# Optimization experiments

Measured on AMD Instinct MI355X. Metric: run time of the kernel, lower is better.

Reference implementation:

```python
import jax, jax.numpy as jnp
import numpy as np

B, N, F, E, D, H, L = 4, 2048, 2, 16, 32, 4, 2
GRAPH_LAYERS = 3
FLOW_ITERS = 10
COST_C = 1.0        # quadratic cost: c*x^2, inv_derivative(y) = y/(2c)
BIG_NUMBER = 1e7


def setup_inputs():
    key = jax.random.key(0)
    ks = jax.random.split(key, 20)
    node_features = jax.random.normal(ks[0], (B, N, F), jnp.float32)
    node_embeddings = jax.random.normal(ks[1], (B, N, E), jnp.float32)
    demands = jax.random.normal(ks[2], (B, N, 1), jnp.float32)
    demands = demands - demands.mean(axis=1, keepdims=True)  # flow conservation
    adj = (jax.random.uniform(ks[3], (B, N, N)) < 0.01).astype(jnp.float32)
    adj = adj * (1.0 - jnp.eye(N, dtype=jnp.float32))
    eye = jnp.broadcast_to(jnp.eye(N, dtype=jnp.float32), (B, N, N))
    neighborhoods = jnp.stack([eye, adj], axis=1)  # [B,L,N,N] hop-0 and hop-1
    def g(k, shape):
        return jax.random.normal(k, shape, jnp.float32) * 0.1
    params = {
        'We1': g(ks[4], (E + F, D)), 'be1': jnp.zeros((D,), jnp.float32),
        'We2': g(ks[5], (D, D)), 'be2': jnp.zeros((D,), jnp.float32),
        'w_attn': g(ks[6], (H, D)),
        'Wo': g(ks[7], (D, D)), 'bo': jnp.zeros((D,), jnp.float32),
        'Wz': g(ks[8], (D, D)), 'Uz': g(ks[9], (D, D)), 'bz': jnp.zeros((D,), jnp.float32),
        'Wr': g(ks[10], (D, D)), 'Ur': g(ks[11], (D, D)), 'br': jnp.zeros((D,), jnp.float32),
        'Wh': g(ks[12], (D, D)), 'Uh': g(ks[13], (D, D)), 'bh': jnp.zeros((D,), jnp.float32),
        'Wd1': g(ks[14], (D, D)), 'bd1': jnp.zeros((D,), jnp.float32),
        'Wd2': g(ks[15], (D, 1)), 'bd2': jnp.zeros((1,), jnp.float32),
        'Wv1': g(ks[16], (D, D)), 'bv1': jnp.zeros((D,), jnp.float32),
        'Wv2': g(ks[17], (D, 1)), 'bv2': jnp.zeros((1,), jnp.float32),
    }
    return {'node_features': node_features, 'node_embeddings': node_embeddings,
            'demands': demands, 'adj': adj, 'neighborhoods': neighborhoods, **params}


def _forward(node_features, node_embeddings, demands, adj, neighborhoods,
             We1, be1, We2, be2, w_attn, Wo, bo,
             Wz, Uz, bz, Wr, Ur, br, Wh, Uh, bh,
             Wd1, bd1, Wd2, bd2, Wv1, bv1, Wv2, bv2):
    # --- node encoder MLP (tanh, activate_final=True) ---
    x = jnp.concatenate([node_embeddings, node_features], axis=-1)   # [B,N,E+F]
    enc = jnp.tanh(jnp.tanh(x @ We1 + be1) @ We2 + be2)               # [B,N,D]
    # row-normalized neighborhood operators (degree-normalized aggregation)
    Mnorm = neighborhoods / (jnp.sum(neighborhoods, axis=-1, keepdims=True) + 1.0)
    # --- graph_layers x (attention neighborhood + GRU state update) ---
    for _ in range(GRAPH_LAYERS):
        agg = jnp.einsum('blnm,bmd->blnd', Mnorm, enc)                # [B,L,N,D]
        scores = jnp.einsum('blnd,hd->bhnl', jnp.tanh(agg), w_attn)   # [B,H,N,L]
        alpha = jax.nn.softmax(scores, axis=-1)
        ctx = jnp.einsum('bhnl,blnd->bnd', alpha, agg) / H            # mean over heads
        nbr = jnp.tanh(ctx @ Wo + bo)                                 # [B,N,D]
        z = jax.nn.sigmoid(nbr @ Wz + enc @ Uz + bz)
        r = jax.nn.sigmoid(nbr @ Wr + enc @ Ur + br)
        h = jnp.tanh(nbr @ Wh + (r * enc) @ Uh + bh)
        enc = z * enc + (1.0 - z) * h
    # --- primal: edge weights, masked softmax, proportional flow solver ---
    pred = (enc @ Wd1 + bd1) @ Wd2 + bd2                              # [B,N,1]
    pw = pred * jnp.transpose(pred, (0, 2, 1))                        # [B,N,N]
    weights = -BIG_NUMBER * (1.0 - adj) + pw
    fwp = jax.nn.softmax(weights, axis=-1)                            # rows sum to 1
    flow0 = fwp * jax.nn.relu(-demands)

    def step(flow, _):
        inflow = jnp.sum(flow, axis=1)[..., None]                     # [B,N,1]
        return fwp * jax.nn.relu(inflow - demands), None

    flow, _ = jax.lax.scan(step, flow0, None, length=FLOW_ITERS)
    flow_cost = jnp.sum(COST_C * flow * flow, axis=(1, 2))            # [B]
    # --- dual: dual variables, dual flows via inverse cost derivative ---
    dual = (enc @ Wv1 + bv1) @ Wv2 + bv2                              # [B,N,1]
    dd = dual - jnp.transpose(dual, (0, 2, 1))                        # [B,N,N]
    df = adj * jax.nn.relu(dd / (2.0 * COST_C))
    dual_cost = jnp.sum(COST_C * df * df - dd * df, axis=(1, 2)) \
        - jnp.sum(dual * demands, axis=(1, 2))                        # [B]
    return flow_cost - dual_cost                                      # primal-dual gap loss, [B]


def reference(node_features, node_embeddings, demands, adj, neighborhoods,
              We1, be1, We2, be2, w_attn, Wo, bo,
              Wz, Uz, bz, Wr, Ur, br, Wh, Uh, bh,
              Wd1, bd1, Wd2, bd2, Wv1, bv1, Wv2, bv2):
    return _forward(node_features, node_embeddings, demands, adj, neighborhoods,
                    We1, be1, We2, be2, w_attn, Wo, bo,
                    Wz, Uz, bz, Wr, Ur, br, Wh, Uh, bh,
                    Wd1, bd1, Wd2, bd2, Wv1, bv1, Wv2, bv2)
```

## Files before the change

kernel.cpp:

```cpp
#include <hip/hip_runtime.h>

#define NN 2048
#define NB 4
#define BN (NB * NN)
#define MAXD 96

__device__ __forceinline__ float fast_rcp(float x) { return __builtin_amdgcn_rcpf(x); }
__device__ __forceinline__ float fast_tanh(float x) {
    float a = __expf(2.0f * fabsf(x));
    float r = 1.0f - 2.0f * fast_rcp(1.0f + a);
    return copysignf(r, x);
}
__device__ __forceinline__ float fast_sigmoid(float x) {
    return fast_rcp(1.0f + __expf(-x));
}

__global__ __launch_bounds__(256) void k_front(
    const float* __restrict__ feat, const float* __restrict__ emb,
    const float* __restrict__ We1, const float* __restrict__ be1,
    const float* __restrict__ We2, const float* __restrict__ be2,
    float* __restrict__ enc_out,
    const float* __restrict__ adj, int* __restrict__ deg, int* __restrict__ cols,
    int* __restrict__ tdeg)
{
    int tid = threadIdx.x;
    if (blockIdx.x < 1024) {
        __shared__ float sW1[18 * 32], sb1[32], sW2[32 * 32], sb2[32];
        for (int i = tid; i < 18 * 32; i += 256) sW1[i] = We1[i];
        for (int i = tid; i < 32 * 32; i += 256) sW2[i] = We2[i];
        if (tid < 32) { sb1[tid] = be1[tid]; sb2[tid] = be2[tid]; }
        __syncthreads();
        int group = tid >> 5, j = tid & 31;
        int node = blockIdx.x * 8 + group;
        float x;
        if (j < 16)      x = emb[node * 16 + j];
        else if (j < 18) x = feat[node * 2 + (j - 16)];
        else             x = 0.f;
        float acc = sb1[j];
#pragma unroll
        for (int k = 0; k < 18; k++)
            acc += __shfl(x, k, 32) * sW1[k * 32 + j];
        float h = fast_tanh(acc);
        float acc2 = sb2[j];
#pragma unroll
        for (int k = 0; k < 32; k++)
            acc2 += __shfl(h, k, 32) * sW2[k * 32 + j];
        enc_out[node * 32 + j] = fast_tanh(acc2);
    } else {
        int wave = tid >> 6, lane = tid & 63;
        int row = (blockIdx.x - 1024) * 4 + wave;
        const float4* p = (const float4*)(adj + (size_t)row * NN);
        int cnt = 0;
        int base = row * MAXD;
#pragma unroll
        for (int it = 0; it < 8; it++) {
            float4 v = p[it * 64 + lane];
            float va[4] = { v.x, v.y, v.z, v.w };
#pragma unroll
            for (int c = 0; c < 4; c++) {
                unsigned long long m = __ballot(va[c] != 0.f);
                if (va[c] != 0.f) {
                    int pos = cnt + __popcll(m & ((1ull << lane) - 1ull));
                    if (pos < MAXD) cols[base + pos] = it * 256 + lane * 4 + c;
                }
                cnt += __popcll(m);
            }
        }
        if (lane == 0) {
            deg[row] = cnt < MAXD ? cnt : MAXD;
            tdeg[row] = 0;
        }
    }
}

__device__ __forceinline__ float layer_rest(
    int g, int j, float e, float a1raw, int d,
    const float4* sPack, const float2* sWhUh, const float* sWo,
    const float* sAttn, const float* sbo, const float* sbz,
    const float* sbr, const float* sbh,
    float2 (*sNE)[32], float (*sCtx)[32])
{
    float agg0 = 0.5f * e;
    float a1 = a1raw * fast_rcp((float)(d + 1));
    float t0 = fast_tanh(agg0), t1 = fast_tanh(a1);
    float td = t0 - t1;
    float s0 = sAttn[j] * td, s1 = sAttn[32 + j] * td,
          s2 = sAttn[64 + j] * td, s3 = sAttn[96 + j] * td;
#pragma unroll
    for (int off = 16; off >= 1; off >>= 1) {
        s0 += __shfl_xor(s0, off, 32);
        s1 += __shfl_xor(s1, off, 32);
        s2 += __shfl_xor(s2, off, 32);
        s3 += __shfl_xor(s3, off, 32);
    }
    float c0 = 0.25f * (fast_sigmoid(s0) + fast_sigmoid(s1) +
                        fast_sigmoid(s2) + fast_sigmoid(s3));
    float ctx = c0 * agg0 + (1.0f - c0) * a1;
    sCtx[g][j] = ctx;
    float acc = sbo[j];
#pragma unroll
    for (int k = 0; k < 32; k++)
        acc += sCtx[g][k] * sWo[k * 32 + j];
    float nbr = fast_tanh(acc);
    sNE[g][j] = make_float2(nbr, e);
    float az = sbz[j], ar = sbr[j];
#pragma unroll
    for (int k = 0; k < 32; k++) {
        float2 ne = sNE[g][k];
        float4 w  = sPack[k * 32 + j];
        az += ne.x * w.x + ne.y * w.y;
        ar += ne.x * w.z + ne.y * w.w;
    }
    float z = fast_sigmoid(az), r = fast_sigmoid(ar);
    sNE[g][j].y = r * e;
    float ah = sbh[j];
#pragma unroll
    for (int k = 0; k < 32; k++) {
        float2 ne = sNE[g][k];
        float2 wh = sWhUh[k * 32 + j];
        ah += ne.x * wh.x + ne.y * wh.y;
    }
    float hc = fast_tanh(ah);
    return z * e + (1.0f - z) * hc;
}

__device__ __forceinline__ float hop1_gather(
    int g, int j, int d, const int* __restrict__ cp,
    const float* __restrict__ encB, int (*sCols)[64])
{
    sCols[g][j]      = cp[j];
    sCols[g][j + 32] = cp[j + 32];
    float a = 0.f, b = 0.f, c = 0.f, e4 = 0.f;
    int i = 0;
    for (; i + 3 < d; i += 4) {
        int m0 = sCols[g][i],     m1 = sCols[g][i + 1];
        int m2 = sCols[g][i + 2], m3 = sCols[g][i + 3];
        a  += encB[m0 * 32 + j];
        b  += encB[m1 * 32 + j];
        c  += encB[m2 * 32 + j];
        e4 += encB[m3 * 32 + j];
    }
    for (; i < d; i++) a += encB[sCols[g][i] * 32 + j];
    return (a + b) + (c + e4);
}

__global__ __launch_bounds__(1024) void k_layer(
    const float* __restrict__ enc_in, float* __restrict__ enc_out,
    const int* __restrict__ deg, const int* __restrict__ cols,
    const float* __restrict__ w_attn,
    const float* __restrict__ Wo, const float* __restrict__ bo,
    const float* __restrict__ Wz, const float* __restrict__ Uz, const float* __restrict__ bz,
    const float* __restrict__ Wr, const float* __restrict__ Ur, const float* __restrict__ br,
    const float* __restrict__ Wh, const float* __restrict__ Uh, const float* __restrict__ bh)
{
    __shared__ float4 sPack[1024];
    __shared__ float2 sWhUh[1024];
    __shared__ float  sWo[1024];
    __shared__ float  sAttn[128], sbo[32], sbz[32], sbr[32], sbh[32];
    __shared__ int    sCols[32][64];
    __shared__ float2 sNE[32][32];
    __shared__ float  sCtx[32][32];
    int tid = threadIdx.x;
    sPack[tid] = make_float4(Wz[tid], Uz[tid], Wr[tid], Ur[tid]);
    sWhUh[tid] = make_float2(Wh[tid], Uh[tid]);
    sWo[tid] = Wo[tid];
    if (tid < 128) sAttn[tid] = w_attn[tid];
    if (tid < 32) { sbo[tid] = bo[tid]; sbz[tid] = bz[tid]; sbr[tid] = br[tid]; sbh[tid] = bh[tid]; }
    int g = tid >> 5, j = tid & 31;
    int node = blockIdx.x * 32 + g;
    int b = node >> 11;
    const float* encB = enc_in + (size_t)(b * NN) * 32;
    float e = enc_in[node * 32 + j];
    int d = deg[node];
    const int* cp = cols + node * MAXD;
    float a1 = hop1_gather(g, j, d, cp, encB, sCols);
    __syncthreads();
    float eo = layer_rest(g, j, e, a1, d, sPack, sWhUh, sWo,
                          sAttn, sbo, sbz, sbr, sbh, sNE, sCtx);
    enc_out[node * 32 + j] = eo;
}

__global__ __launch_bounds__(1024) void k_layer_last(
    const float* __restrict__ enc_in,
    const int* __restrict__ deg, const int* __restrict__ cols,
    const float* __restrict__ w_attn,
    const float* __restrict__ Wo, const float* __restrict__ bo,
    const float* __restrict__ Wz, const float* __restrict__ Uz, const float* __restrict__ bz,
    const float* __restrict__ Wr, const float* __restrict__ Ur, const float* __restrict__ br,
    const float* __restrict__ Wh, const float* __restrict__ Uh, const float* __restrict__ bh,
    const float* __restrict__ Wd1, const float* __restrict__ bd1,
    const float* __restrict__ Wd2, const float* __restrict__ bd2,
    const float* __restrict__ Wv1, const float* __restrict__ bv1,
    const float* __restrict__ Wv2, const float* __restrict__ bv2,
    float* __restrict__ pred, float* __restrict__ dual)
{
    __shared__ float4 sPack[1024];
    __shared__ float2 sWhUh[1024];
    __shared__ float  sWo[1024];
    __shared__ float  sAttn[128], sbo[32], sbz[32], sbr[32], sbh[32];
    __shared__ float  swd[32], swv[32], shc[2];
    __shared__ int    sCols[32][64];
    __shared__ float2 sNE[32][32];
    __shared__ float  sCtx[32][32];
    int tid = threadIdx.x;
    sPack[tid] = make_float4(Wz[tid], Uz[tid], Wr[tid], Ur[tid]);
    sWhUh[tid] = make_float2(Wh[tid], Uh[tid]);
    sWo[tid] = Wo[tid];
    if (tid < 128) sAttn[tid] = w_attn[tid];
    if (tid < 32) { sbo[tid] = bo[tid]; sbz[tid] = bz[tid]; sbr[tid] = br[tid]; sbh[tid] = bh[tid]; }
    if (tid >= 64 && tid < 96) {
        int k = tid - 64;
        float a = 0.f, av = 0.f;
#pragma unroll
        for (int jj = 0; jj < 32; jj++) {
            a  += Wd1[k * 32 + jj] * Wd2[jj];
            av += Wv1[k * 32 + jj] * Wv2[jj];
        }
        swd[k] = a; swv[k] = av;
    }
    if (tid == 96) {
        float c1 = 0.f, c2 = 0.f;
#pragma unroll
        for (int jj = 0; jj < 32; jj++) {
            c1 += bd1[jj] * Wd2[jj];
            c2 += bv1[jj] * Wv2[jj];
        }
        shc[0] = c1 + bd2[0]; shc[1] = c2 + bv2[0];
    }
    int g = tid >> 5, j = tid & 31;
    int node = blockIdx.x * 32 + g;
    int b = node >> 11;
    const float* encB = enc_in + (size_t)(b * NN) * 32;
    float e = enc_in[node * 32 + j];
    int d = deg[node];
    const int* cp = cols + node * MAXD;
    float a1 = hop1_gather(g, j, d, cp, encB, sCols);
    __syncthreads();
    float eo = layer_rest(g, j, e, a1, d, sPack, sWhUh, sWo,
                          sAttn, sbo, sbz, sbr, sbh, sNE, sCtx);
    float pd = eo * swd[j];
    float dv = eo * swv[j];
#pragma unroll
    for (int off = 16; off >= 1; off >>= 1) {
        pd += __shfl_xor(pd, off, 32);
        dv += __shfl_xor(dv, off, 32);
    }
    if (j == 0) {
        pred[node] = pd + shc[0];
        dual[node] = dv + shc[1];
    }
}

__global__ __launch_bounds__(256) void k_edge_scatter(
    const int* __restrict__ deg, const int* __restrict__ cols,
    const float* __restrict__ pred, const float* __restrict__ dual,
    int* __restrict__ tdeg, unsigned* __restrict__ tpack,
    float* __restrict__ rowsq, float* __restrict__ rowdual)
{
    int wave = threadIdx.x >> 6, lane = threadIdx.x & 63;
    int row = blockIdx.x * 4 + wave;
    int b = row >> 11;
    int rloc = row & (NN - 1);
    const float* predB = pred + b * NN;
    const float* dualB = dual + b * NN;
    int d = deg[row];
    int base = row * MAXD;
    float pn = pred[row];
    float dn = dual[row];
    if (d <= 64) {
        int c = 0;
        float w = -1e30f, du = 0.f;
        bool act = lane < d;
        if (act) {
            c = cols[base + lane];
            w = pn * predB[c];
            float dd = dn - dualB[c];
            if (dd > 0.f) du = -0.25f * dd * dd;
        }
        float mx = w;
#pragma unroll
        for (int off = 32; off >= 1; off >>= 1) mx = fmaxf(mx, __shfl_xor(mx, off));
        float ex = act ? __expf(w - mx) : 0.f;
        float den = ex;
#pragma unroll
        for (int off = 32; off >= 1; off >>= 1) { den += __shfl_xor(den, off); du += __shfl_xor(du, off); }
        float f = ex * fast_rcp(den);
        float rs = f * f;
        if (act) {
            int pos = atomicAdd(&tdeg[b * NN + c], 1);
            if (pos < MAXD) {
                unsigned wv = ((__float_as_uint(f) + 0x400u) & 0xFFFFF800u) | (unsigned)rloc;
                tpack[(size_t)(b * MAXD + pos) * NN + c] = wv;
            }
        } else rs = 0.f;
#pragma unroll
        for (int off = 32; off >= 1; off >>= 1) rs += __shfl_xor(rs, off);
        if (lane == 0) { rowsq[row] = rs; rowdual[row] = du; }
    } else {
        float mx = -1e30f;
        for (int i = lane; i < d; i += 64) {
            int c = cols[base + i];
            mx = fmaxf(mx, pn * predB[c]);
        }
#pragma unroll
        for (int off = 32; off >= 1; off >>= 1) mx = fmaxf(mx, __shfl_xor(mx, off));
        float den = 0.f, du = 0.f;
        for (int i = lane; i < d; i += 64) {
            int c = cols[base + i];
            den += __expf(pn * predB[c] - mx);
            float dd = dn - dualB[c];
            if (dd > 0.f) du -= 0.25f * dd * dd;
        }
#pragma unroll
        for (int off = 32; off >= 1; off >>= 1) { den += __shfl_xor(den, off); du += __shfl_xor(du, off); }
        float invden = fast_rcp(den);
        float rs = 0.f;
        for (int i = lane; i < d; i += 64) {
            int c = cols[base + i];
            float f = __expf(pn * predB[c] - mx) * invden;
            rs += f * f;
            int pos = atomicAdd(&tdeg[b * NN + c], 1);
            if (pos < MAXD) {
                unsigned wv = ((__float_as_uint(f) + 0x400u) & 0xFFFFF800u) | (unsigned)rloc;
                tpack[(size_t)(b * MAXD + pos) * NN + c] = wv;
            }
        }
#pragma unroll
        for (int off = 32; off >= 1; off >>= 1) rs += __shfl_xor(rs, off);
        if (lane == 0) { rowsq[row] = rs; rowdual[row] = du; }
    }
}

__global__ __launch_bounds__(1024) void k_flow_batch(
    const int* __restrict__ tdeg, const unsigned* __restrict__ tpack,
    const float* __restrict__ demands,
    const float* __restrict__ rowsq, const float* __restrict__ rowdual,
    const float* __restrict__ dual, float* __restrict__ out)
{
    __shared__ float sdem[NN], sA[NN], sBuf[NN];
    __shared__ float red[3][16];
    int tid = threadIdx.x;
    int b = blockIdx.x;
    const float* demB = demands + b * NN;
    for (int n = tid; n < NN; n += 1024) {
        float dm = demB[n];
        sdem[n] = dm;
        sA[n] = fmaxf(-dm, 0.f);
    }
    __syncthreads();
    int n0 = tid, n1 = tid + 1024;
    int d0 = tdeg[b * NN + n0];
    int d1 = tdeg[b * NN + n1];
    if (d0 > MAXD) d0 = MAXD;
    if (d1 > MAXD) d1 = MAXD;
    float dm0 = sdem[n0], dm1 = sdem[n1];
    const unsigned* tp = tpack + (size_t)b * MAXD * NN;
#pragma unroll 1
    for (int it = 0; it < 5; it++) {
        {
            float a0 = 0.f, a1 = 0.f;
            for (int i = 0; i < d0; i++) {
                unsigned wv = tp[i * NN + n0];
                a0 += __uint_as_float(wv & 0xFFFFF800u) * sA[wv & 0x7FFu];
            }
            for (int i = 0; i < d1; i++) {
                unsigned wv = tp[i * NN + n1];
                a1 += __uint_as_float(wv & 0xFFFFF800u) * sA[wv & 0x7FFu];
            }
            sBuf[n0] = fmaxf(a0 - dm0, 0.f);
            sBuf[n1] = fmaxf(a1 - dm1, 0.f);
        }
        __syncthreads();
        {
            float a0 = 0.f, a1 = 0.f;
            for (int i = 0; i < d0; i++) {
                unsigned wv = tp[i * NN + n0];
                a0 += __uint_as_float(wv & 0xFFFFF800u) * sBuf[wv & 0x7FFu];
            }
            for (int i = 0; i < d1; i++) {
                unsigned wv = tp[i * NN + n1];
                a1 += __uint_as_float(wv & 0xFFFFF800u) * sBuf[wv & 0x7FFu];
            }
            sA[n0] = fmaxf(a0 - dm0, 0.f);
            sA[n1] = fmaxf(a1 - dm1, 0.f);
        }
        __syncthreads();
    }
    float fc = 0.f, ds = 0.f, dq = 0.f;
    for (int n = tid; n < NN; n += 1024) {
        int row = b * NN + n;
        float sv = sA[n];
        fc += rowsq[row] * sv * sv;
        ds += rowdual[row];
        dq += dual[row] * sdem[n];
    }
#pragma unroll
    for (int off = 32; off >= 1; off >>= 1) {
        fc += __shfl_xor(fc, off);
        ds += __shfl_xor(ds, off);
        dq += __shfl_xor(dq, off);
    }
    int wv = tid >> 6;
    if ((tid & 63) == 0) { red[0][wv] = fc; red[1][wv] = ds; red[2][wv] = dq; }
    __syncthreads();
    if (tid == 0) {
        float a = 0.f, s1 = 0.f, s2 = 0.f;
        for (int w = 0; w < 16; w++) { a += red[0][w]; s1 += red[1][w]; s2 += red[2][w]; }
        out[b] = a - s1 + s2;
    }
}

extern "C" void kernel_launch(void* const* d_in, const int* in_sizes, int n_in,
                              void* d_out, int out_size, void* d_ws, size_t ws_size,
                              hipStream_t stream) {
    const float* feat = (const float*)d_in[0];
    const float* emb  = (const float*)d_in[1];
    const float* dem  = (const float*)d_in[2];
    const float* adj  = (const float*)d_in[3];
    const float* We1 = (const float*)d_in[5];
    const float* be1 = (const float*)d_in[6];
    const float* We2 = (const float*)d_in[7];
    const float* be2 = (const float*)d_in[8];
    const float* w_attn = (const float*)d_in[9];
    const float* Wo = (const float*)d_in[10];
    const float* bo = (const float*)d_in[11];
    const float* Wz = (const float*)d_in[12];
    const float* Uz = (const float*)d_in[13];
    const float* bz = (const float*)d_in[14];
    const float* Wr = (const float*)d_in[15];
    const float* Ur = (const float*)d_in[16];
    const float* br = (const float*)d_in[17];
    const float* Wh = (const float*)d_in[18];
    const float* Uh = (const float*)d_in[19];
    const float* bh = (const float*)d_in[20];
    const float* Wd1 = (const float*)d_in[21];
    const float* bd1 = (const float*)d_in[22];
    const float* Wd2 = (const float*)d_in[23];
    const float* bd2 = (const float*)d_in[24];
    const float* Wv1 = (const float*)d_in[25];
    const float* bv1 = (const float*)d_in[26];
    const float* Wv2 = (const float*)d_in[27];
    const float* bv2 = (const float*)d_in[28];
    float* out = (float*)d_out;

    float* w = (float*)d_ws;
    float* enc0 = w;            w += (size_t)BN * 32;
    float* enc1 = w;            w += (size_t)BN * 32;
    int*   degp = (int*)w;      w += BN;
    int*   colp = (int*)w;      w += (size_t)BN * MAXD;
    float* pred = w;            w += BN;
    float* dual = w;            w += BN;
    float* rowsq = w;           w += BN;
    float* rowdual = w;         w += BN;
    int*   tdeg = (int*)w;      w += BN;
    unsigned* tpk = (unsigned*)w; w += (size_t)BN * MAXD;

    k_front<<<3072, 256, 0, stream>>>(feat, emb, We1, be1, We2, be2, enc0,
                                      adj, degp, colp, tdeg);
    k_layer<<<BN / 32, 1024, 0, stream>>>(enc0, enc1, degp, colp, w_attn,
                                          Wo, bo, Wz, Uz, bz, Wr, Ur, br, Wh, Uh, bh);
    k_layer<<<BN / 32, 1024, 0, stream>>>(enc1, enc0, degp, colp, w_attn,
                                          Wo, bo, Wz, Uz, bz, Wr, Ur, br, Wh, Uh, bh);
    k_layer_last<<<BN / 32, 1024, 0, stream>>>(enc0, degp, colp, w_attn,
                                               Wo, bo, Wz, Uz, bz, Wr, Ur, br, Wh, Uh, bh,
                                               Wd1, bd1, Wd2, bd2, Wv1, bv1, Wv2, bv2,
                                               pred, dual);
    k_edge_scatter<<<BN / 4, 256, 0, stream>>>(degp, colp, pred, dual,
                                               tdeg, tpk, rowsq, rowdual);
    k_flow_batch<<<NB, 1024, 0, stream>>>(tdeg, tpk, dem,
                                          rowsq, rowdual, dual, out);
}
```

Measured before the change: 381.2 us.

## Sort flow-iteration nodes by in-degree to balance warps; vectorize GRU LDS reads

Adds a per-batch kernel that counts each node's in-degree, bucket-sorts nodes by it, and stores a permutation, rank and sorted degree. The transposed edge pack is written in rank order, so each wavefront in the sequential flow iteration handles nodes of similar degree. This is meant to cut divergence from uneven loop trip counts in the single-block-per-batch flow kernel, which sits on the critical path. Separately, the GRU/attention matvecs now read two LDS entries per load using float2/float4. The cost is one extra launch that does shared-memory atomics, plus an extra rank lookup in the scatter.

```diff
diff --git a/kernel.cpp b/kernel.cpp
--- a/kernel.cpp
+++ b/kernel.cpp
@@ -73,6 +73,44 @@
     }
 }
 
+__global__ __launch_bounds__(1024) void k_perm(
+    const int* __restrict__ deg, const int* __restrict__ cols,
+    int* __restrict__ perm, int* __restrict__ rank, int* __restrict__ degS)
+{
+    __shared__ int sIndeg[NN];
+    __shared__ int sHist[MAXD + 1];
+    __shared__ int sOff[MAXD + 1];
+    int tid = threadIdx.x, b = blockIdx.x;
+    for (int n = tid; n < NN; n += 1024) sIndeg[n] = 0;
+    if (tid <= MAXD) sHist[tid] = 0;
+    __syncthreads();
+    for (int r = tid; r < NN; r += 1024) {
+        int row = b * NN + r;
+        int d = deg[row];
+        const int* cp = cols + row * MAXD;
+        for (int i = 0; i < d; i++) atomicAdd(&sIndeg[cp[i]], 1);
+    }
+    __syncthreads();
+    for (int n = tid; n < NN; n += 1024) {
+        int dg = sIndeg[n]; if (dg > MAXD) dg = MAXD;
+        sIndeg[n] = dg;
+        atomicAdd(&sHist[dg], 1);
+    }
+    __syncthreads();
+    if (tid == 0) {
+        int acc = 0;
+        for (int i = 0; i <= MAXD; i++) { sOff[i] = acc; acc += sHist[i]; }
+    }
+    __syncthreads();
+    for (int n = tid; n < NN; n += 1024) {
+        int dg = sIndeg[n];
+        int r = atomicAdd(&sOff[dg], 1);
+        perm[b * NN + r] = n;
+        rank[b * NN + n] = r;
+        degS[b * NN + r] = dg;
+    }
+}
+
 __device__ __forceinline__ float layer_rest(
     int g, int j, float e, float a1raw, int d,
     const float4* sPack, const float2* sWhUh, const float* sWo,
@@ -99,26 +137,30 @@
     sCtx[g][j] = ctx;
     float acc = sbo[j];
 #pragma unroll
-    for (int k = 0; k < 32; k++)
-        acc += sCtx[g][k] * sWo[k * 32 + j];
+    for (int k = 0; k < 32; k += 2) {
+        float2 c2 = *(const float2*)&sCtx[g][k];
+        acc += c2.x * sWo[k * 32 + j] + c2.y * sWo[(k + 1) * 32 + j];
+    }
     float nbr = fast_tanh(acc);
     sNE[g][j] = make_float2(nbr, e);
     float az = sbz[j], ar = sbr[j];
 #pragma unroll
-    for (int k = 0; k < 32; k++) {
-        float2 ne = sNE[g][k];
-        float4 w  = sPack[k * 32 + j];
-        az += ne.x * w.x + ne.y * w.y;
-        ar += ne.x * w.z + ne.y * w.w;
+    for (int k = 0; k < 32; k += 2) {
+        float4 ne2 = *(const float4*)&sNE[g][k];
+        float4 w0  = sPack[k * 32 + j];
+        float4 w1  = sPack[(k + 1) * 32 + j];
+        az += ne2.x * w0.x + ne2.y * w0.y + ne2.z * w1.x + ne2.w * w1.y;
+        ar += ne2.x * w0.z + ne2.y * w0.w + ne2.z * w1.z + ne2.w * w1.w;
     }
     float z = fast_sigmoid(az), r = fast_sigmoid(ar);
     sNE[g][j].y = r * e;
     float ah = sbh[j];
 #pragma unroll
-    for (int k = 0; k < 32; k++) {
-        float2 ne = sNE[g][k];
-        float2 wh = sWhUh[k * 32 + j];
-        ah += ne.x * wh.x + ne.y * wh.y;
+    for (int k = 0; k < 32; k += 2) {
+        float4 ne2 = *(const float4*)&sNE[g][k];
+        float2 w0 = sWhUh[k * 32 + j];
+        float2 w1 = sWhUh[(k + 1) * 32 + j];
+        ah += ne2.x * w0.x + ne2.y * w0.y + ne2.z * w1.x + ne2.w * w1.y;
     }
     float hc = fast_tanh(ah);
     return z * e + (1.0f - z) * hc;
@@ -158,8 +200,8 @@
     __shared__ float  sWo[1024];
     __shared__ float  sAttn[128], sbo[32], sbz[32], sbr[32], sbh[32];
     __shared__ int    sCols[32][64];
-    __shared__ float2 sNE[32][32];
-    __shared__ float  sCtx[32][32];
+    __shared__ __align__(16) float2 sNE[32][32];
+    __shared__ __align__(16) float  sCtx[32][32];
     int tid = threadIdx.x;
     sPack[tid] = make_float4(Wz[tid], Uz[tid], Wr[tid], Ur[tid]);
     sWhUh[tid] = make_float2(Wh[tid], Uh[tid]);
@@ -200,8 +242,8 @@
     __shared__ float  sAttn[128], sbo[32], sbz[32], sbr[32], sbh[32];
     __shared__ float  swd[32], swv[32], shc[2];
     __shared__ int    sCols[32][64];
-    __shared__ float2 sNE[32][32];
-    __shared__ float  sCtx[32][32];
+    __shared__ __align__(16) float2 sNE[32][32];
+    __shared__ __align__(16) float  sCtx[32][32];
     int tid = threadIdx.x;
     sPack[tid] = make_float4(Wz[tid], Uz[tid], Wr[tid], Ur[tid]);
     sWhUh[tid] = make_float2(Wh[tid], Uh[tid]);
@@ -254,6 +296,7 @@
 __global__ __launch_bounds__(256) void k_edge_scatter(
     const int* __restrict__ deg, const int* __restrict__ cols,
     const float* __restrict__ pred, const float* __restrict__ dual,
+    const int* __restrict__ rank,
     int* __restrict__ tdeg, unsigned* __restrict__ tpack,
     float* __restrict__ rowsq, float* __restrict__ rowdual)
 {
@@ -289,8 +332,9 @@
         if (act) {
             int pos = atomicAdd(&tdeg[b * NN + c], 1);
             if (pos < MAXD) {
+                int rk = rank[b * NN + c];
                 unsigned wv = ((__float_as_uint(f) + 0x400u) & 0xFFFFF800u) | (unsigned)rloc;
-                tpack[(size_t)(b * MAXD + pos) * NN + c] = wv;
+                tpack[(size_t)(b * MAXD + pos) * NN + rk] = wv;
             }
         } else rs = 0.f;
 #pragma unroll
@@ -321,8 +365,9 @@
             rs += f * f;
             int pos = atomicAdd(&tdeg[b * NN + c], 1);
             if (pos < MAXD) {
+                int rk = rank[b * NN + c];
                 unsigned wv = ((__float_as_uint(f) + 0x400u) & 0xFFFFF800u) | (unsigned)rloc;
-                tpack[(size_t)(b * MAXD + pos) * NN + c] = wv;
+                tpack[(size_t)(b * MAXD + pos) * NN + rk] = wv;
             }
         }
 #pragma unroll
@@ -332,7 +377,8 @@
 }
 
 __global__ __launch_bounds__(1024) void k_flow_batch(
-    const int* __restrict__ tdeg, const unsigned* __restrict__ tpack,
+    const int* __restrict__ perm, const int* __restrict__ degS,
+    const unsigned* __restrict__ tpack,
     const float* __restrict__ demands,
     const float* __restrict__ rowsq, const float* __restrict__ rowdual,
     const float* __restrict__ dual, float* __restrict__ out)
@@ -348,41 +394,41 @@
         sA[n] = fmaxf(-dm, 0.f);
     }
     __syncthreads();
-    int n0 = tid, n1 = tid + 1024;
-    int d0 = tdeg[b * NN + n0];
-    int d1 = tdeg[b * NN + n1];
-    if (d0 > MAXD) d0 = MAXD;
-    if (d1 > MAXD) d1 = MAXD;
-    float dm0 = sdem[n0], dm1 = sdem[n1];
+    int q0 = tid, q1 = tid + 1024;
+    int m0 = perm[b * NN + q0];
+    int m1 = perm[b * NN + q1];
+    int d0 = degS[b * NN + q0];
+    int d1 = degS[b * NN + q1];
+    float dm0 = sdem[m0], dm1 = sdem[m1];
     const unsigned* tp = tpack + (size_t)b * MAXD * NN;
 #pragma unroll 1
     for (int it = 0; it < 5; it++) {
         {
             float a0 = 0.f, a1 = 0.f;
             for (int i = 0; i < d0; i++) {
-                unsigned wv = tp[i * NN + n0];
+                unsigned wv = tp[i * NN + q0];
                 a0 += __uint_as_float(wv & 0xFFFFF800u) * sA[wv & 0x7FFu];
             }
             for (int i = 0; i < d1; i++) {
-                unsigned wv = tp[i * NN + n1];
+                unsigned wv = tp[i * NN + q1];
                 a1 += __uint_as_float(wv & 0xFFFFF800u) * sA[wv & 0x7FFu];
             }
-            sBuf[n0] = fmaxf(a0 - dm0, 0.f);
-            sBuf[n1] = fmaxf(a1 - dm1, 0.f);
+            sBuf[m0] = fmaxf(a0 - dm0, 0.f);
+            sBuf[m1] = fmaxf(a1 - dm1, 0.f);
         }
         __syncthreads();
         {
             float a0 = 0.f, a1 = 0.f;
             for (int i = 0; i < d0; i++) {
-                unsigned wv = tp[i * NN + n0];
+                unsigned wv = tp[i * NN + q0];
                 a0 += __uint_as_float(wv & 0xFFFFF800u) * sBuf[wv & 0x7FFu];
             }
             for (int i = 0; i < d1; i++) {
-                unsigned wv = tp[i * NN + n1];
+                unsigned wv = tp[i * NN + q1];
                 a1 += __uint_as_float(wv & 0xFFFFF800u) * sBuf[wv & 0x7FFu];
             }
-            sA[n0] = fmaxf(a0 - dm0, 0.f);
-            sA[n1] = fmaxf(a1 - dm1, 0.f);
+            sA[m0] = fmaxf(a0 - dm0, 0.f);
+            sA[m1] = fmaxf(a1 - dm1, 0.f);
         }
         __syncthreads();
     }
@@ -453,10 +499,14 @@
     float* rowsq = w;           w += BN;
     float* rowdual = w;         w += BN;
     int*   tdeg = (int*)w;      w += BN;
+    int*   permp = (int*)w;     w += BN;
+    int*   rankp = (int*)w;     w += BN;
+    int*   degSp = (int*)w;     w += BN;
     unsigned* tpk = (unsigned*)w; w += (size_t)BN * MAXD;
 
     k_front<<<3072, 256, 0, stream>>>(feat, emb, We1, be1, We2, be2, enc0,
                                       adj, degp, colp, tdeg);
+    k_perm<<<NB, 1024, 0, stream>>>(degp, colp, permp, rankp, degSp);
     k_layer<<<BN / 32, 1024, 0, stream>>>(enc0, enc1, degp, colp, w_attn,
                                           Wo, bo, Wz, Uz, bz, Wr, Ur, br, Wh, Uh, bh);
     k_layer<<<BN / 32, 1024, 0, stream>>>(enc1, enc0, degp, colp, w_attn,
@@ -465,8 +515,8 @@
                                                Wo, bo, Wz, Uz, bz, Wr, Ur, br, Wh, Uh, bh,
                                                Wd1, bd1, Wd2, bd2, Wv1, bv1, Wv2, bv2,
                                                pred, dual);
-    k_edge_scatter<<<BN / 4, 256, 0, stream>>>(degp, colp, pred, dual,
+    k_edge_scatter<<<BN / 4, 256, 0, stream>>>(degp, colp, pred, dual, rankp,
                                                tdeg, tpk, rowsq, rowdual);
-    k_flow_batch<<<NB, 1024, 0, stream>>>(tdeg, tpk, dem,
+    k_flow_batch<<<NB, 1024, 0, stream>>>(permp, degSp, tpk, dem,
                                           rowsq, rowdual, dual, out);
 }
```

Result: slower. 399.8 us (+4.9%).
